# Kernel tuning notes

Hardware: AMD Instinct MI355X
Metric: run time of the kernel (lower is better)

## Reference

```python
import jax, jax.numpy as jnp
import numpy as np

N = 100000      # num nodes
E = 800000      # num edges
IN = 256        # in_features
D = 64          # out_features per head
H = 4           # num_heads
EF = 64         # edge_feats
NET = 8         # num_etype
SLOPE = 0.2     # leaky relu negative slope


def setup_inputs() -> dict:
    key = jax.random.key(0)
    ks = jax.random.split(key, 12)
    s = 0.05
    h = jax.random.normal(ks[0], (N, IN), jnp.float32)
    row = jax.random.randint(ks[1], (E,), 0, N, dtype=jnp.int32)   # src
    col = jax.random.randint(ks[2], (E,), 0, N, dtype=jnp.int32)   # dst
    tp = jax.random.randint(ks[3], (E,), 0, NET, dtype=jnp.int32)  # edge type
    W = jax.random.normal(ks[4], (IN, D * H), jnp.float32) * s
    W_e = jax.random.normal(ks[5], (EF, EF * H), jnp.float32) * s
    edge_emb = jax.random.normal(ks[6], (NET, EF), jnp.float32) * s
    a_l = jax.random.normal(ks[7], (1, H, D), jnp.float32) * s
    a_r = jax.random.normal(ks[8], (1, H, D), jnp.float32) * s
    a_e = jax.random.normal(ks[9], (1, H, EF), jnp.float32) * s
    res_W = jax.random.normal(ks[10], (IN, D * H), jnp.float32) * s
    res_b = jnp.zeros((D * H,), jnp.float32)
    return {"h": h, "W": W, "W_e": W_e, "edge_emb": edge_emb,
            "a_l": a_l, "a_r": a_r, "a_e": a_e,
            "res_W": res_W, "res_b": res_b,
            "row": row, "col": col, "tp": tp}


def reference(h, W, W_e, edge_emb, a_l, a_r, a_e, res_W, res_b, row, col, tp):
    # node projection -> [N, H, D]; nan-guard as in the original
    emb = jnp.nan_to_num((h @ W).reshape(-1, H, D), nan=0.0)
    # edge-type embedding projection -> [NET, H, EF]
    e = (edge_emb @ W_e).reshape(-1, H, EF)
    # per-edge attention logits [E, H]
    h_l = (a_l * emb).sum(-1)[row]
    h_r = (a_r * emb).sum(-1)[col]
    h_e = (a_e * e).sum(-1)[tp]
    att = jax.nn.leaky_relu(h_l + h_r + h_e, SLOPE)
    # segment softmax over edges grouped by destination node
    m = jax.ops.segment_max(att, col, num_segments=N)          # [N, H]
    ex = jnp.exp(att - m[col])                                 # [E, H]
    denom = jax.ops.segment_sum(ex, col, num_segments=N)      # [N, H]
    alpha = ex / denom[col]                                    # [E, H]
    # gather-multiply-scatter message passing: [E, H, D] -> [N, H, D]
    msg = emb[row] * alpha[:, :, None]
    out = jax.ops.segment_sum(msg, col, num_segments=N).reshape(N, H * D)
    # residual linear + elu activation
    out = out + h @ res_W + res_b
    return jax.nn.elu(out)
```

## Files before the change

### kernel.cpp

```cpp
#include <hip/hip_runtime.h>

#define N_NODES 100000
#define E_EDGES 800000
#define IN_F 256
#define D_HEAD 64
#define H_HEADS 4
#define EF_F 64
#define NET_T 8
#define HD 256
#define SLOPE 0.2f

typedef unsigned short u16;
typedef unsigned long long u64;
typedef __attribute__((ext_vector_type(8))) short bf16x8;
typedef __attribute__((ext_vector_type(4))) float f32x4;

static __device__ __forceinline__ u16 f2bf(float f) {
    unsigned int u = __float_as_uint(f);
    unsigned int r = u + 0x7FFFu + ((u >> 16) & 1u);
    return (u16)(r >> 16);
}
static __device__ __forceinline__ float bf2f(unsigned int u) {
    return __uint_as_float(u << 16);
}

__global__ void k_se(const float* __restrict__ edge_emb, const float* __restrict__ W_e,
                     const float* __restrict__ a_e, float* __restrict__ s_e) {
    int tid = threadIdx.x;
    int t  = tid >> 5;
    int h  = (tid >> 3) & 3;
    int fc = tid & 7;
    float part = 0.f;
    for (int j = 0; j < 8; ++j) {
        int f = fc * 8 + j;
        float acc = 0.f;
        for (int k = 0; k < EF_F; ++k)
            acc += edge_emb[t * EF_F + k] * W_e[k * (EF_F * H_HEADS) + h * EF_F + f];
        part += a_e[h * EF_F + f] * acc;
    }
    for (int off = 1; off < 8; off <<= 1)
        part += __shfl_xor(part, off, 64);
    if (fc == 0) s_e[t * H_HEADS + h] = part;
}

__global__ void k_prep_w(const float* __restrict__ W, const float* __restrict__ resW,
                         u16* __restrict__ Bfrag) {
    const int gid = blockIdx.x * 256 + threadIdx.x;
    const int lane = gid & 63;
    const int fragid = gid >> 6;
    const int n = fragid & 3;
    const int ks = (fragid >> 2) & 7;
    const int g = fragid >> 5;
    const int c = g * 64 + n * 16 + (lane & 15);
    const int k0 = ks * 32 + (lane >> 4) * 8;
    const float* src = (c < HD) ? &W[c] : &resW[c - HD];
    u16 tmp[8];
#pragma unroll
    for (int j = 0; j < 8; ++j)
        tmp[j] = f2bf(src[(size_t)(k0 + j) * HD]);
    *reinterpret_cast<uint4*>(&Bfrag[(size_t)fragid * 512 + lane * 8]) =
        *reinterpret_cast<const uint4*>(tmp);
}

__global__ __launch_bounds__(512, 2)
void k_mfma(const float* __restrict__ A, const u16* __restrict__ Bfrag,
            const float* __restrict__ a_l, const float* __restrict__ a_r,
            const float* __restrict__ resb,
            u16* __restrict__ emb_bf, float* __restrict__ s_l, float* __restrict__ s_r,
            float* __restrict__ outp) {
    __shared__ char At[32768];
    const int tid = threadIdx.x;
    const int lane = tid & 63;
    const int wid = tid >> 6;
    const int row0 = blockIdx.x * 64;

#pragma unroll
    for (int c = 0; c < 8; ++c) {
        const int lin8 = c * 4096 + tid * 8;
        const int r_lin = lin8 >> 9;
        int grow = row0 + r_lin;
        if (grow >= N_NODES) grow = N_NODES - 1;
        const int colb = lin8 & 511;
        const float4 v = *reinterpret_cast<const float4*>(&A[(size_t)grow * IN_F + (colb >> 1)]);
        uint2 o;
        o.x = (unsigned)f2bf(v.x) | ((unsigned)f2bf(v.y) << 16);
        o.y = (unsigned)f2bf(v.z) | ((unsigned)f2bf(v.w) << 16);
        *reinterpret_cast<uint2*>(&At[lin8 ^ ((r_lin & 7) << 4)]) = o;
    }
    __syncthreads();

    const int lr = lane & 15;
    const int lg = lane >> 4;
    const int xr = (lr & 7) << 4;
    const int klg = lg * 16;

    int rowbase[4];
#pragma unroll
    for (int m = 0; m < 4; ++m) rowbase[m] = (m * 16 + lr) * 512;

    const u16* bp = Bfrag + (size_t)wid * 16384 + lane * 8;

    f32x4 acc[4][4] = {};
#pragma unroll
    for (int ks = 0; ks < 8; ++ks) {
        bf16x8 af[4], bfr[4];
        const int kx = ((ks << 6) + klg) ^ xr;
#pragma unroll
        for (int n = 0; n < 4; ++n)
            bfr[n] = *reinterpret_cast<const bf16x8*>(&bp[ks * 2048 + n * 512]);
#pragma unroll
        for (int m = 0; m < 4; ++m)
            af[m] = *reinterpret_cast<const bf16x8*>(&At[rowbase[m] + kx]);
#pragma unroll
        for (int m = 0; m < 4; ++m)
#pragma unroll
            for (int n = 0; n < 4; ++n)
                acc[m][n] = __builtin_amdgcn_mfma_f32_16x16x32_bf16(bfr[n], af[m], acc[m][n], 0, 0, 0);
    }

    if (wid < 4) {
        const int h = wid;
        float4 alv[4], arv[4];
#pragma unroll
        for (int n = 0; n < 4; ++n) {
            alv[n] = *reinterpret_cast<const float4*>(&a_l[h * D_HEAD + n * 16 + lg * 4]);
            arv[n] = *reinterpret_cast<const float4*>(&a_r[h * D_HEAD + n * 16 + lg * 4]);
        }
#pragma unroll
        for (int m = 0; m < 4; ++m) {
            const int node = row0 + m * 16 + lr;
            float dl = 0.f, dr = 0.f;
            u64 pk[4];
#pragma unroll
            for (int n = 0; n < 4; ++n) {
                float v0 = acc[m][n][0], v1 = acc[m][n][1], v2 = acc[m][n][2], v3 = acc[m][n][3];
                v0 = isnan(v0) ? 0.f : v0;
                v1 = isnan(v1) ? 0.f : v1;
                v2 = isnan(v2) ? 0.f : v2;
                v3 = isnan(v3) ? 0.f : v3;
                dl += v0 * alv[n].x + v1 * alv[n].y + v2 * alv[n].z + v3 * alv[n].w;
                dr += v0 * arv[n].x + v1 * arv[n].y + v2 * arv[n].z + v3 * arv[n].w;
                pk[n] = (u64)f2bf(v0) | ((u64)f2bf(v1) << 16) |
                        ((u64)f2bf(v2) << 32) | ((u64)f2bf(v3) << 48);
            }
            if (node < N_NODES) {
                const size_t base = (size_t)node * HD + h * D_HEAD + lg * 4;
#pragma unroll
                for (int n = 0; n < 4; ++n)
                    *reinterpret_cast<u64*>(&emb_bf[base + n * 16]) = pk[n];
            }
            dl += __shfl_xor(dl, 16, 64); dr += __shfl_xor(dr, 16, 64);
            dl += __shfl_xor(dl, 32, 64); dr += __shfl_xor(dr, 32, 64);
            if (lg == 0 && node < N_NODES) {
                s_l[node * H_HEADS + h] = dl;
                s_r[node * H_HEADS + h] = dr;
            }
        }
    } else {
        const int c0 = (wid - 4) * 64 + lg * 4;
        float4 rb[4];
#pragma unroll
        for (int n = 0; n < 4; ++n)
            rb[n] = *reinterpret_cast<const float4*>(&resb[c0 + n * 16]);
#pragma unroll
        for (int m = 0; m < 4; ++m) {
            const int node = row0 + m * 16 + lr;
            if (node < N_NODES) {
                const size_t base = (size_t)node * HD + c0;
#pragma unroll
                for (int n = 0; n < 4; ++n) {
                    float4 o;
                    o.x = acc[m][n][0] + rb[n].x;
                    o.y = acc[m][n][1] + rb[n].y;
                    o.z = acc[m][n][2] + rb[n].z;
                    o.w = acc[m][n][3] + rb[n].w;
                    *reinterpret_cast<float4*>(&outp[base + n * 16]) = o;
                }
            }
        }
    }
}

__global__ void k_hist(const int* __restrict__ col, int* __restrict__ counts) {
    int e = blockIdx.x * 256 + threadIdx.x;
    if (e < E_EDGES) atomicAdd(&counts[col[e]], 1);
}

__global__ void k_scan1(const int* __restrict__ counts, int* __restrict__ row_ptr,
                        int* __restrict__ partials) {
    __shared__ int sd[256];
    const int t = threadIdx.x, b = blockIdx.x;
    const int base = b * 1024 + t * 4;
    int v[4];
#pragma unroll
    for (int j = 0; j < 4; ++j) v[j] = (base + j < N_NODES) ? counts[base + j] : 0;
    const int s = v[0] + v[1] + v[2] + v[3];
    sd[t] = s;
    __syncthreads();
    for (int off = 1; off < 256; off <<= 1) {
        int y = (t >= off) ? sd[t - off] : 0;
        __syncthreads();
        sd[t] += y;
        __syncthreads();
    }
    int p = sd[t] - s;
#pragma unroll
    for (int j = 0; j < 4; ++j) {
        if (base + j < N_NODES) row_ptr[base + j] = p;
        p += v[j];
    }
    if (t == 255) partials[b] = sd[255];
}

__global__ void k_scan2(int* __restrict__ partials) {
    __shared__ int sd[128];
    const int t = threadIdx.x;
    const int v = (t < 98) ? partials[t] : 0;
    sd[t] = v;
    __syncthreads();
    for (int off = 1; off < 128; off <<= 1) {
        int y = (t >= off) ? sd[t - off] : 0;
        __syncthreads();
        sd[t] += y;
        __syncthreads();
    }
    if (t < 98) partials[t] = sd[t] - v;
}

__global__ void k_scan3(int* __restrict__ row_ptr, int* __restrict__ fill,
                        const int* __restrict__ partials) {
    const int i = blockIdx.x * 256 + threadIdx.x;
    if (i < N_NODES) {
        const int v = row_ptr[i] + partials[i >> 10];
        row_ptr[i] = v;
        fill[i] = v;
    }
    if (i == 0) row_ptr[N_NODES] = E_EDGES;
}

__global__ void k_scatter(const int* __restrict__ row, const int* __restrict__ col,
                          const int* __restrict__ tp, int* __restrict__ fill,
                          int* __restrict__ perm) {
    int e = blockIdx.x * 256 + threadIdx.x;
    if (e < E_EDGES) {
        int c = col[e];
        int p = atomicAdd(&fill[c], 1);
        perm[p] = row[e] | (tp[e] << 20);
    }
}

__global__ __launch_bounds__(256)
void k_aggregate(const int* __restrict__ row_ptr, const int* __restrict__ perm,
                 const u16* __restrict__ emb_bf, const float* __restrict__ s_l,
                 const float* __restrict__ s_r, const float* __restrict__ s_e,
                 float* __restrict__ outp) {
    const int wave = threadIdx.x >> 6;
    const int lane = threadIdx.x & 63;
    const int n = blockIdx.x * 4 + wave;
    const int h = lane >> 4;
    const int start = row_ptr[n], end = row_ptr[n + 1];
    const float srh = s_r[n * H_HEADS + h];
    const size_t o = (size_t)n * HD + lane * 4;
    const float4 res = *reinterpret_cast<const float4*>(&outp[o]);

    float se_h[NET_T];
#pragma unroll
    for (int t = 0; t < NET_T; ++t) se_h[t] = s_e[t * H_HEADS + h];

    float a0 = 0.f, a1 = 0.f, a2 = 0.f, a3 = 0.f, den = 0.f;
    int i = start;
    for (; i + 4 <= end; i += 4) {
        const int p0 = perm[i], p1 = perm[i + 1], p2 = perm[i + 2], p3 = perm[i + 3];
        const int r0 = p0 & 0xFFFFF, r1 = p1 & 0xFFFFF, r2 = p2 & 0xFFFFF, r3 = p3 & 0xFFFFF;
        const u64 ev0 = *reinterpret_cast<const u64*>(&emb_bf[(size_t)r0 * HD + lane * 4]);
        const u64 ev1 = *reinterpret_cast<const u64*>(&emb_bf[(size_t)r1 * HD + lane * 4]);
        const u64 ev2 = *reinterpret_cast<const u64*>(&emb_bf[(size_t)r2 * HD + lane * 4]);
        const u64 ev3 = *reinterpret_cast<const u64*>(&emb_bf[(size_t)r3 * HD + lane * 4]);
        const float sl0 = s_l[r0 * H_HEADS + h];
        const float sl1 = s_l[r1 * H_HEADS + h];
        const float sl2 = s_l[r2 * H_HEADS + h];
        const float sl3 = s_l[r3 * H_HEADS + h];
        float lg0 = sl0 + srh + se_h[p0 >> 20];
        float lg1 = sl1 + srh + se_h[p1 >> 20];
        float lg2 = sl2 + srh + se_h[p2 >> 20];
        float lg3 = sl3 + srh + se_h[p3 >> 20];
        lg0 = (lg0 > 0.f) ? lg0 : SLOPE * lg0;
        lg1 = (lg1 > 0.f) ? lg1 : SLOPE * lg1;
        lg2 = (lg2 > 0.f) ? lg2 : SLOPE * lg2;
        lg3 = (lg3 > 0.f) ? lg3 : SLOPE * lg3;
        const float ex0 = __expf(lg0), ex1 = __expf(lg1);
        const float ex2 = __expf(lg2), ex3 = __expf(lg3);
        a0 += ex0 * bf2f((unsigned)(ev0) & 0xFFFFu)       + ex1 * bf2f((unsigned)(ev1) & 0xFFFFu)
            + ex2 * bf2f((unsigned)(ev2) & 0xFFFFu)       + ex3 * bf2f((unsigned)(ev3) & 0xFFFFu);
        a1 += ex0 * bf2f((unsigned)(ev0 >> 16) & 0xFFFFu) + ex1 * bf2f((unsigned)(ev1 >> 16) & 0xFFFFu)
            + ex2 * bf2f((unsigned)(ev2 >> 16) & 0xFFFFu) + ex3 * bf2f((unsigned)(ev3 >> 16) & 0xFFFFu);
        a2 += ex0 * bf2f((unsigned)(ev0 >> 32) & 0xFFFFu) + ex1 * bf2f((unsigned)(ev1 >> 32) & 0xFFFFu)
            + ex2 * bf2f((unsigned)(ev2 >> 32) & 0xFFFFu) + ex3 * bf2f((unsigned)(ev3 >> 32) & 0xFFFFu);
        a3 += ex0 * bf2f((unsigned)(ev0 >> 48) & 0xFFFFu) + ex1 * bf2f((unsigned)(ev1 >> 48) & 0xFFFFu)
            + ex2 * bf2f((unsigned)(ev2 >> 48) & 0xFFFFu) + ex3 * bf2f((unsigned)(ev3 >> 48) & 0xFFFFu);
        den += ex0 + ex1 + ex2 + ex3;
    }
    for (; i < end; ++i) {
        const int p0 = perm[i];
        const int r0 = p0 & 0xFFFFF;
        const u64 ev0 = *reinterpret_cast<const u64*>(&emb_bf[(size_t)r0 * HD + lane * 4]);
        float lg0 = s_l[r0 * H_HEADS + h] + srh + se_h[p0 >> 20];
        lg0 = (lg0 > 0.f) ? lg0 : SLOPE * lg0;
        const float ex0 = __expf(lg0);
        a0 += ex0 * bf2f((unsigned)(ev0) & 0xFFFFu);
        a1 += ex0 * bf2f((unsigned)(ev0 >> 16) & 0xFFFFu);
        a2 += ex0 * bf2f((unsigned)(ev0 >> 32) & 0xFFFFu);
        a3 += ex0 * bf2f((unsigned)(ev0 >> 48) & 0xFFFFu);
        den += ex0;
    }
    const float inv = (den > 0.f) ? 1.f / den : 0.f;
    float4 out;
    float x;
    x = a0 * inv + res.x; out.x = (x > 0.f) ? x : expm1f(x);
    x = a1 * inv + res.y; out.y = (x > 0.f) ? x : expm1f(x);
    x = a2 * inv + res.z; out.z = (x > 0.f) ? x : expm1f(x);
    x = a3 * inv + res.w; out.w = (x > 0.f) ? x : expm1f(x);
    *reinterpret_cast<float4*>(&outp[o]) = out;
}

extern "C" void kernel_launch(void* const* d_in, const int* in_sizes, int n_in,
                              void* d_out, int out_size, void* d_ws, size_t ws_size,
                              hipStream_t stream) {
    const float* h    = (const float*)d_in[0];
    const float* W    = (const float*)d_in[1];
    const float* W_e  = (const float*)d_in[2];
    const float* eemb = (const float*)d_in[3];
    const float* a_l  = (const float*)d_in[4];
    const float* a_r  = (const float*)d_in[5];
    const float* a_e  = (const float*)d_in[6];
    const float* resW = (const float*)d_in[7];
    const float* resb = (const float*)d_in[8];
    const int* row = (const int*)d_in[9];
    const int* col = (const int*)d_in[10];
    const int* tp  = (const int*)d_in[11];
    float* outp = (float*)d_out;

    char* ws = (char*)d_ws;
    size_t off = 0;
    auto alloc = [&](size_t b) { size_t o = off; off += (b + 255) & ~(size_t)255; return o; };
    u16*  Bfrag   = (u16*)(ws + alloc((size_t)512 * IN_F * 2));
    u16*  emb_bf  = (u16*)(ws + alloc((size_t)N_NODES * HD * 2));
    float* s_l    = (float*)(ws + alloc((size_t)N_NODES * H_HEADS * 4));
    float* s_r    = (float*)(ws + alloc((size_t)N_NODES * H_HEADS * 4));
    float* s_e    = (float*)(ws + alloc(NET_T * H_HEADS * 4));
    int*  counts  = (int*)(ws + alloc((size_t)N_NODES * 4));
    int*  row_ptr = (int*)(ws + alloc((size_t)(N_NODES + 1) * 4));
    int*  fill    = (int*)(ws + alloc((size_t)N_NODES * 4));
    int*  perm    = (int*)(ws + alloc((size_t)E_EDGES * 4));
    int*  partials= (int*)(ws + alloc(128 * 4));

    k_se<<<1, 256, 0, stream>>>(eemb, W_e, a_e, s_e);
    k_prep_w<<<64, 256, 0, stream>>>(W, resW, Bfrag);
    k_mfma<<<(N_NODES + 63) / 64, 512, 0, stream>>>(h, Bfrag, a_l, a_r, resb, emb_bf, s_l, s_r, outp);
    hipMemsetAsync(counts, 0, (size_t)N_NODES * 4, stream);
    k_hist<<<(E_EDGES + 255) / 256, 256, 0, stream>>>(col, counts);
    k_scan1<<<98, 256, 0, stream>>>(counts, row_ptr, partials);
    k_scan2<<<1, 128, 0, stream>>>(partials);
    k_scan3<<<(N_NODES + 255) / 256, 256, 0, stream>>>(row_ptr, fill, partials);
    k_scatter<<<(E_EDGES + 255) / 256, 256, 0, stream>>>(row, col, tp, fill, perm);
    k_aggregate<<<N_NODES / 4, 256, 0, stream>>>(row_ptr, perm, emb_bf, s_l, s_r, s_e, outp);
}
```

Baseline: 322.6 us.

## Make MFMA GEMM persistent with register-resident B, precompute edge exp weights

The projection GEMM becomes a persistent kernel (512 blocks, occupancy hint lowered to 1) that loads all B fragments into registers once and loops over row tiles. A new per-edge kernel computes the leaky-relu exponentials for all four heads in edge order. The aggregation kernel then reads a 64-bit (row, edge id) permutation and gathers those weights instead of recomputing logits from s_l, s_r and s_e. The ELU tail uses a fast exp instead of expm1f. The cost is an extra 12.8 MB exw buffer, a wider permutation, and a scattered gather of exw in the aggregation loop.

New measurement: 365.9 us. 13.4% more time.

```diff
diff --git a/kernel.cpp b/kernel.cpp
--- a/kernel.cpp
+++ b/kernel.cpp
@@ -9,6 +9,7 @@
 #define NET_T 8
 #define HD 256
 #define SLOPE 0.2f
+#define NTILES ((N_NODES + 63) / 64)
 
 typedef unsigned short u16;
 typedef unsigned long long u64;
@@ -62,7 +63,7 @@
         *reinterpret_cast<const uint4*>(tmp);
 }
 
-__global__ __launch_bounds__(512, 2)
+__global__ __launch_bounds__(512, 1)
 void k_mfma(const float* __restrict__ A, const u16* __restrict__ Bfrag,
             const float* __restrict__ a_l, const float* __restrict__ a_r,
             const float* __restrict__ resb,
@@ -72,113 +73,137 @@
     const int tid = threadIdx.x;
     const int lane = tid & 63;
     const int wid = tid >> 6;
-    const int row0 = blockIdx.x * 64;
-
-#pragma unroll
-    for (int c = 0; c < 8; ++c) {
-        const int lin8 = c * 4096 + tid * 8;
-        const int r_lin = lin8 >> 9;
-        int grow = row0 + r_lin;
-        if (grow >= N_NODES) grow = N_NODES - 1;
-        const int colb = lin8 & 511;
-        const float4 v = *reinterpret_cast<const float4*>(&A[(size_t)grow * IN_F + (colb >> 1)]);
-        uint2 o;
-        o.x = (unsigned)f2bf(v.x) | ((unsigned)f2bf(v.y) << 16);
-        o.y = (unsigned)f2bf(v.z) | ((unsigned)f2bf(v.w) << 16);
-        *reinterpret_cast<uint2*>(&At[lin8 ^ ((r_lin & 7) << 4)]) = o;
-    }
-    __syncthreads();
-
     const int lr = lane & 15;
     const int lg = lane >> 4;
     const int xr = (lr & 7) << 4;
     const int klg = lg * 16;
 
+    const u16* bp = Bfrag + (size_t)wid * 16384 + lane * 8;
+    bf16x8 bfr[8][4];
+#pragma unroll
+    for (int ks = 0; ks < 8; ++ks)
+#pragma unroll
+        for (int n = 0; n < 4; ++n)
+            bfr[ks][n] = *reinterpret_cast<const bf16x8*>(&bp[ks * 2048 + n * 512]);
+
     int rowbase[4];
 #pragma unroll
     for (int m = 0; m < 4; ++m) rowbase[m] = (m * 16 + lr) * 512;
 
-    const u16* bp = Bfrag + (size_t)wid * 16384 + lane * 8;
-
-    f32x4 acc[4][4] = {};
-#pragma unroll
-    for (int ks = 0; ks < 8; ++ks) {
-        bf16x8 af[4], bfr[4];
-        const int kx = ((ks << 6) + klg) ^ xr;
-#pragma unroll
-        for (int n = 0; n < 4; ++n)
-            bfr[n] = *reinterpret_cast<const bf16x8*>(&bp[ks * 2048 + n * 512]);
-#pragma unroll
-        for (int m = 0; m < 4; ++m)
-            af[m] = *reinterpret_cast<const bf16x8*>(&At[rowbase[m] + kx]);
-#pragma unroll
-        for (int m = 0; m < 4; ++m)
+    for (int tile = blockIdx.x; tile < NTILES; tile += gridDim.x) {
+        const int row0 = tile * 64;
+        __syncthreads();
+#pragma unroll
+        for (int c = 0; c < 8; ++c) {
+            const int lin8 = c * 4096 + tid * 8;
+            const int r_lin = lin8 >> 9;
+            int grow = row0 + r_lin;
+            if (grow >= N_NODES) grow = N_NODES - 1;
+            const int colb = lin8 & 511;
+            const float4 v = *reinterpret_cast<const float4*>(&A[(size_t)grow * IN_F + (colb >> 1)]);
+            uint2 o;
+            o.x = (unsigned)f2bf(v.x) | ((unsigned)f2bf(v.y) << 16);
+            o.y = (unsigned)f2bf(v.z) | ((unsigned)f2bf(v.w) << 16);
+            *reinterpret_cast<uint2*>(&At[lin8 ^ ((r_lin & 7) << 4)]) = o;
+        }
+        __syncthreads();
+
+        f32x4 acc[4][4] = {};
+#pragma unroll
+        for (int ks = 0; ks < 8; ++ks) {
+            bf16x8 af[4];
+            const int kx = ((ks << 6) + klg) ^ xr;
+#pragma unroll
+            for (int m = 0; m < 4; ++m)
+                af[m] = *reinterpret_cast<const bf16x8*>(&At[rowbase[m] + kx]);
+#pragma unroll
+            for (int m = 0; m < 4; ++m)
+#pragma unroll
+                for (int n = 0; n < 4; ++n)
+                    acc[m][n] = __builtin_amdgcn_mfma_f32_16x16x32_bf16(bfr[ks][n], af[m], acc[m][n], 0, 0, 0);
+        }
+
+        if (wid < 4) {
+            const int h = wid;
+            float4 alv[4], arv[4];
+#pragma unroll
+            for (int n = 0; n < 4; ++n) {
+                alv[n] = *reinterpret_cast<const float4*>(&a_l[h * D_HEAD + n * 16 + lg * 4]);
+                arv[n] = *reinterpret_cast<const float4*>(&a_r[h * D_HEAD + n * 16 + lg * 4]);
+            }
+#pragma unroll
+            for (int m = 0; m < 4; ++m) {
+                const int node = row0 + m * 16 + lr;
+                float dl = 0.f, dr = 0.f;
+                u64 pk[4];
+#pragma unroll
+                for (int n = 0; n < 4; ++n) {
+                    float v0 = acc[m][n][0], v1 = acc[m][n][1], v2 = acc[m][n][2], v3 = acc[m][n][3];
+                    v0 = isnan(v0) ? 0.f : v0;
+                    v1 = isnan(v1) ? 0.f : v1;
+                    v2 = isnan(v2) ? 0.f : v2;
+                    v3 = isnan(v3) ? 0.f : v3;
+                    dl += v0 * alv[n].x + v1 * alv[n].y + v2 * alv[n].z + v3 * alv[n].w;
+                    dr += v0 * arv[n].x + v1 * arv[n].y + v2 * arv[n].z + v3 * arv[n].w;
+                    pk[n] = (u64)f2bf(v0) | ((u64)f2bf(v1) << 16) |
+                            ((u64)f2bf(v2) << 32) | ((u64)f2bf(v3) << 48);
+                }
+                if (node < N_NODES) {
+                    const size_t base = (size_t)node * HD + h * D_HEAD + lg * 4;
+#pragma unroll
+                    for (int n = 0; n < 4; ++n)
+                        *reinterpret_cast<u64*>(&emb_bf[base + n * 16]) = pk[n];
+                }
+                dl += __shfl_xor(dl, 16, 64); dr += __shfl_xor(dr, 16, 64);
+                dl += __shfl_xor(dl, 32, 64); dr += __shfl_xor(dr, 32, 64);
+                if (lg == 0 && node < N_NODES) {
+                    s_l[node * H_HEADS + h] = dl;
+                    s_r[node * H_HEADS + h] = dr;
+                }
+            }
+        } else {
+            const int c0 = (wid - 4) * 64 + lg * 4;
+            float4 rb[4];
 #pragma unroll
             for (int n = 0; n < 4; ++n)
-                acc[m][n] = __builtin_amdgcn_mfma_f32_16x16x32_bf16(bfr[n], af[m], acc[m][n], 0, 0, 0);
-    }
-
-    if (wid < 4) {
-        const int h = wid;
-        float4 alv[4], arv[4];
-#pragma unroll
-        for (int n = 0; n < 4; ++n) {
-            alv[n] = *reinterpret_cast<const float4*>(&a_l[h * D_HEAD + n * 16 + lg * 4]);
-            arv[n] = *reinterpret_cast<const float4*>(&a_r[h * D_HEAD + n * 16 + lg * 4]);
-        }
-#pragma unroll
-        for (int m = 0; m < 4; ++m) {
-            const int node = row0 + m * 16 + lr;
-            float dl = 0.f, dr = 0.f;
-            u64 pk[4];
-#pragma unroll
-            for (int n = 0; n < 4; ++n) {
-                float v0 = acc[m][n][0], v1 = acc[m][n][1], v2 = acc[m][n][2], v3 = acc[m][n][3];
-                v0 = isnan(v0) ? 0.f : v0;
-                v1 = isnan(v1) ? 0.f : v1;
-                v2 = isnan(v2) ? 0.f : v2;
-                v3 = isnan(v3) ? 0.f : v3;
-                dl += v0 * alv[n].x + v1 * alv[n].y + v2 * alv[n].z + v3 * alv[n].w;
-                dr += v0 * arv[n].x + v1 * arv[n].y + v2 * arv[n].z + v3 * arv[n].w;
-                pk[n] = (u64)f2bf(v0) | ((u64)f2bf(v1) << 16) |
-                        ((u64)f2bf(v2) << 32) | ((u64)f2bf(v3) << 48);
-            }
-            if (node < N_NODES) {
-                const size_t base = (size_t)node * HD + h * D_HEAD + lg * 4;
-#pragma unroll
-                for (int n = 0; n < 4; ++n)
-                    *reinterpret_cast<u64*>(&emb_bf[base + n * 16]) = pk[n];
-            }
-            dl += __shfl_xor(dl, 16, 64); dr += __shfl_xor(dr, 16, 64);
-            dl += __shfl_xor(dl, 32, 64); dr += __shfl_xor(dr, 32, 64);
-            if (lg == 0 && node < N_NODES) {
-                s_l[node * H_HEADS + h] = dl;
-                s_r[node * H_HEADS + h] = dr;
-            }
-        }
-    } else {
-        const int c0 = (wid - 4) * 64 + lg * 4;
-        float4 rb[4];
-#pragma unroll
-        for (int n = 0; n < 4; ++n)
-            rb[n] = *reinterpret_cast<const float4*>(&resb[c0 + n * 16]);
-#pragma unroll
-        for (int m = 0; m < 4; ++m) {
-            const int node = row0 + m * 16 + lr;
-            if (node < N_NODES) {
-                const size_t base = (size_t)node * HD + c0;
-#pragma unroll
-                for (int n = 0; n < 4; ++n) {
-                    float4 o;
-                    o.x = acc[m][n][0] + rb[n].x;
-                    o.y = acc[m][n][1] + rb[n].y;
-                    o.z = acc[m][n][2] + rb[n].z;
-                    o.w = acc[m][n][3] + rb[n].w;
-                    *reinterpret_cast<float4*>(&outp[base + n * 16]) = o;
+                rb[n] = *reinterpret_cast<const float4*>(&resb[c0 + n * 16]);
+#pragma unroll
+            for (int m = 0; m < 4; ++m) {
+                const int node = row0 + m * 16 + lr;
+                if (node < N_NODES) {
+                    const size_t base = (size_t)node * HD + c0;
+#pragma unroll
+                    for (int n = 0; n < 4; ++n) {
+                        float4 o;
+                        o.x = acc[m][n][0] + rb[n].x;
+                        o.y = acc[m][n][1] + rb[n].y;
+                        o.z = acc[m][n][2] + rb[n].z;
+                        o.w = acc[m][n][3] + rb[n].w;
+                        *reinterpret_cast<float4*>(&outp[base + n * 16]) = o;
+                    }
                 }
             }
         }
     }
+}
+
+__global__ void k_edge(const int* __restrict__ row, const int* __restrict__ col,
+                       const int* __restrict__ tp, const float* __restrict__ s_l,
+                       const float* __restrict__ s_r, const float* __restrict__ s_e,
+                       float4* __restrict__ exw) {
+    const int e = blockIdx.x * 256 + threadIdx.x;
+    if (e >= E_EDGES) return;
+    const int r = row[e], c = col[e], t = tp[e];
+    const float4 sl = *reinterpret_cast<const float4*>(&s_l[r * 4]);
+    const float4 sr = *reinterpret_cast<const float4*>(&s_r[c * 4]);
+    const float4 se = *reinterpret_cast<const float4*>(&s_e[t * 4]);
+    float4 ex;
+    float x;
+    x = sl.x + sr.x + se.x; x = (x > 0.f) ? x : SLOPE * x; ex.x = __expf(x);
+    x = sl.y + sr.y + se.y; x = (x > 0.f) ? x : SLOPE * x; ex.y = __expf(x);
+    x = sl.z + sr.z + se.z; x = (x > 0.f) ? x : SLOPE * x; ex.z = __expf(x);
+    x = sl.w + sr.w + se.w; x = (x > 0.f) ? x : SLOPE * x; ex.w = __expf(x);
+    exw[e] = ex;
 }
 
 __global__ void k_hist(const int* __restrict__ col, int* __restrict__ counts) {
@@ -239,57 +264,42 @@
 }
 
 __global__ void k_scatter(const int* __restrict__ row, const int* __restrict__ col,
-                          const int* __restrict__ tp, int* __restrict__ fill,
-                          int* __restrict__ perm) {
+                          int* __restrict__ fill, u64* __restrict__ perm_re) {
     int e = blockIdx.x * 256 + threadIdx.x;
     if (e < E_EDGES) {
         int c = col[e];
         int p = atomicAdd(&fill[c], 1);
-        perm[p] = row[e] | (tp[e] << 20);
+        perm_re[p] = (u64)(unsigned)row[e] | ((u64)(unsigned)e << 32);
     }
 }
 
 __global__ __launch_bounds__(256)
-void k_aggregate(const int* __restrict__ row_ptr, const int* __restrict__ perm,
-                 const u16* __restrict__ emb_bf, const float* __restrict__ s_l,
-                 const float* __restrict__ s_r, const float* __restrict__ s_e,
+void k_aggregate(const int* __restrict__ row_ptr, const u64* __restrict__ perm_re,
+                 const u16* __restrict__ emb_bf, const float* __restrict__ exw,
                  float* __restrict__ outp) {
     const int wave = threadIdx.x >> 6;
     const int lane = threadIdx.x & 63;
     const int n = blockIdx.x * 4 + wave;
     const int h = lane >> 4;
     const int start = row_ptr[n], end = row_ptr[n + 1];
-    const float srh = s_r[n * H_HEADS + h];
     const size_t o = (size_t)n * HD + lane * 4;
     const float4 res = *reinterpret_cast<const float4*>(&outp[o]);
-
-    float se_h[NET_T];
-#pragma unroll
-    for (int t = 0; t < NET_T; ++t) se_h[t] = s_e[t * H_HEADS + h];
 
     float a0 = 0.f, a1 = 0.f, a2 = 0.f, a3 = 0.f, den = 0.f;
     int i = start;
     for (; i + 4 <= end; i += 4) {
-        const int p0 = perm[i], p1 = perm[i + 1], p2 = perm[i + 2], p3 = perm[i + 3];
-        const int r0 = p0 & 0xFFFFF, r1 = p1 & 0xFFFFF, r2 = p2 & 0xFFFFF, r3 = p3 & 0xFFFFF;
+        const u64 q0 = perm_re[i],     q1 = perm_re[i + 1];
+        const u64 q2 = perm_re[i + 2], q3 = perm_re[i + 3];
+        const int r0 = (int)(unsigned)q0, r1 = (int)(unsigned)q1;
+        const int r2 = (int)(unsigned)q2, r3 = (int)(unsigned)q3;
+        const float ex0 = exw[((q0 >> 32) << 2) + h];
+        const float ex1 = exw[((q1 >> 32) << 2) + h];
+        const float ex2 = exw[((q2 >> 32) << 2) + h];
+        const float ex3 = exw[((q3 >> 32) << 2) + h];
         const u64 ev0 = *reinterpret_cast<const u64*>(&emb_bf[(size_t)r0 * HD + lane * 4]);
         const u64 ev1 = *reinterpret_cast<const u64*>(&emb_bf[(size_t)r1 * HD + lane * 4]);
         const u64 ev2 = *reinterpret_cast<const u64*>(&emb_bf[(size_t)r2 * HD + lane * 4]);
         const u64 ev3 = *reinterpret_cast<const u64*>(&emb_bf[(size_t)r3 * HD + lane * 4]);
-        const float sl0 = s_l[r0 * H_HEADS + h];
-        const float sl1 = s_l[r1 * H_HEADS + h];
-        const float sl2 = s_l[r2 * H_HEADS + h];
-        const float sl3 = s_l[r3 * H_HEADS + h];
-        float lg0 = sl0 + srh + se_h[p0 >> 20];
-        float lg1 = sl1 + srh + se_h[p1 >> 20];
-        float lg2 = sl2 + srh + se_h[p2 >> 20];
-        float lg3 = sl3 + srh + se_h[p3 >> 20];
-        lg0 = (lg0 > 0.f) ? lg0 : SLOPE * lg0;
-        lg1 = (lg1 > 0.f) ? lg1 : SLOPE * lg1;
-        lg2 = (lg2 > 0.f) ? lg2 : SLOPE * lg2;
-        lg3 = (lg3 > 0.f) ? lg3 : SLOPE * lg3;
-        const float ex0 = __expf(lg0), ex1 = __expf(lg1);
-        const float ex2 = __expf(lg2), ex3 = __expf(lg3);
         a0 += ex0 * bf2f((unsigned)(ev0) & 0xFFFFu)       + ex1 * bf2f((unsigned)(ev1) & 0xFFFFu)
             + ex2 * bf2f((unsigned)(ev2) & 0xFFFFu)       + ex3 * bf2f((unsigned)(ev3) & 0xFFFFu);
         a1 += ex0 * bf2f((unsigned)(ev0 >> 16) & 0xFFFFu) + ex1 * bf2f((unsigned)(ev1 >> 16) & 0xFFFFu)
@@ -301,12 +311,10 @@
         den += ex0 + ex1 + ex2 + ex3;
     }
     for (; i < end; ++i) {
-        const int p0 = perm[i];
-        const int r0 = p0 & 0xFFFFF;
+        const u64 q0 = perm_re[i];
+        const int r0 = (int)(unsigned)q0;
+        const float ex0 = exw[((q0 >> 32) << 2) + h];
         const u64 ev0 = *reinterpret_cast<const u64*>(&emb_bf[(size_t)r0 * HD + lane * 4]);
-        float lg0 = s_l[r0 * H_HEADS + h] + srh + se_h[p0 >> 20];
-        lg0 = (lg0 > 0.f) ? lg0 : SLOPE * lg0;
-        const float ex0 = __expf(lg0);
         a0 += ex0 * bf2f((unsigned)(ev0) & 0xFFFFu);
         a1 += ex0 * bf2f((unsigned)(ev0 >> 16) & 0xFFFFu);
         a2 += ex0 * bf2f((unsigned)(ev0 >> 32) & 0xFFFFu);
@@ -316,10 +324,10 @@
     const float inv = (den > 0.f) ? 1.f / den : 0.f;
     float4 out;
     float x;
-    x = a0 * inv + res.x; out.x = (x > 0.f) ? x : expm1f(x);
-    x = a1 * inv + res.y; out.y = (x > 0.f) ? x : expm1f(x);
-    x = a2 * inv + res.z; out.z = (x > 0.f) ? x : expm1f(x);
-    x = a3 * inv + res.w; out.w = (x > 0.f) ? x : expm1f(x);
+    x = a0 * inv + res.x; out.x = (x > 0.f) ? x : __expf(x) - 1.f;
+    x = a1 * inv + res.y; out.y = (x > 0.f) ? x : __expf(x) - 1.f;
+    x = a2 * inv + res.z; out.z = (x > 0.f) ? x : __expf(x) - 1.f;
+    x = a3 * inv + res.w; out.w = (x > 0.f) ? x : __expf(x) - 1.f;
     *reinterpret_cast<float4*>(&outp[o]) = out;
 }
 
@@ -351,17 +359,19 @@
     int*  counts  = (int*)(ws + alloc((size_t)N_NODES * 4));
     int*  row_ptr = (int*)(ws + alloc((size_t)(N_NODES + 1) * 4));
     int*  fill    = (int*)(ws + alloc((size_t)N_NODES * 4));
-    int*  perm    = (int*)(ws + alloc((size_t)E_EDGES * 4));
+    u64*  perm_re = (u64*)(ws + alloc((size_t)E_EDGES * 8));
+    float* exw    = (float*)(ws + alloc((size_t)E_EDGES * H_HEADS * 4));
     int*  partials= (int*)(ws + alloc(128 * 4));
 
     k_se<<<1, 256, 0, stream>>>(eemb, W_e, a_e, s_e);
     k_prep_w<<<64, 256, 0, stream>>>(W, resW, Bfrag);
-    k_mfma<<<(N_NODES + 63) / 64, 512, 0, stream>>>(h, Bfrag, a_l, a_r, resb, emb_bf, s_l, s_r, outp);
+    k_mfma<<<512, 512, 0, stream>>>(h, Bfrag, a_l, a_r, resb, emb_bf, s_l, s_r, outp);
     hipMemsetAsync(counts, 0, (size_t)N_NODES * 4, stream);
     k_hist<<<(E_EDGES + 255) / 256, 256, 0, stream>>>(col, counts);
     k_scan1<<<98, 256, 0, stream>>>(counts, row_ptr, partials);
     k_scan2<<<1, 128, 0, stream>>>(partials);
     k_scan3<<<(N_NODES + 255) / 256, 256, 0, stream>>>(row_ptr, fill, partials);
-    k_scatter<<<(E_EDGES + 255) / 256, 256, 0, stream>>>(row, col, tp, fill, perm);
-    k_aggregate<<<N_NODES / 4, 256, 0, stream>>>(row_ptr, perm, emb_bf, s_l, s_r, s_e, outp);
-}
+    k_scatter<<<(E_EDGES + 255) / 256, 256, 0, stream>>>(row, col, fill, perm_re);
+    k_edge<<<(E_EDGES + 255) / 256, 256, 0, stream>>>(row, col, tp, s_l, s_r, s_e, (float4*)exw);
+    k_aggregate<<<N_NODES / 4, 256, 0, stream>>>(row_ptr, perm_re, emb_bf, exw, outp);
+}
```
